# Optimization experiments

Hardware: AMD Instinct MI355X
Metric: run time of the kernel (lower is better)

The kernel has to match this reference:

```python
import jax, jax.numpy as jnp
import numpy as np

N = 20000      # n_nodes
E = 320000     # n_edges (multiple of 4, so _from_coo drops nothing)
D = 512        # embed_dim
H = 8          # num_heads
DK = D // H    # d_k = 64


def setup_inputs() -> dict:
    key = jax.random.key(0)
    ks = jax.random.split(key, 12)
    x = jax.random.normal(ks[0], (N, D), jnp.float32)
    rows = jnp.sort(jax.random.randint(ks[1], (E,), 0, N))
    cols = jax.random.randint(ks[2], (E,), 0, N)
    edge_index = jnp.stack([rows, cols]).astype(jnp.int32)  # [2, E]
    att_bias = jax.random.normal(ks[3], (E, H), jnp.float32)
    s = float(1.0 / np.sqrt(D))  # ~xavier scale
    Wq = jax.random.normal(ks[4], (D, D), jnp.float32) * s
    Wk = jax.random.normal(ks[5], (D, D), jnp.float32) * s
    Wv = jax.random.normal(ks[6], (D, D), jnp.float32) * s
    Wo = jax.random.normal(ks[7], (D, D), jnp.float32) * s
    bq = jnp.zeros((D,), jnp.float32)
    bk = jnp.zeros((D,), jnp.float32)
    bv = jnp.zeros((D,), jnp.float32)
    bo = jnp.zeros((D,), jnp.float32)
    return dict(x=x, edge_index=edge_index, att_bias=att_bias,
                Wq=Wq, bq=bq, Wk=Wk, bk=bk, Wv=Wv, bv=bv, Wo=Wo, bo=bo)


def reference(x, edge_index, att_bias, Wq, bq, Wk, bk, Wv, bv, Wo, bo):
    n = x.shape[0]
    rows, cols = edge_index[0], edge_index[1]
    # per-head projections: [n, H, DK]
    q = (x @ Wq + bq).reshape(n, H, DK)
    k = (x @ Wk + bk).reshape(n, H, DK)
    v = (x @ Wv + bv).reshape(n, H, DK)
    scale = 1.0 / jnp.sqrt(jnp.asarray(DK, x.dtype))
    # masked QK^T on the edge pattern, plus additive bias: [E, H]
    logits = jnp.einsum('ehd,ehd->eh', q[rows] * scale, k[cols]) + att_bias
    # CSR (segment) softmax over each destination row
    row_max = jax.ops.segment_max(logits, rows, num_segments=n)      # [n, H]
    p = jnp.exp(logits - row_max[rows])                              # [E, H]
    denom = jax.ops.segment_sum(p, rows, num_segments=n)            # [n, H]
    att = p / denom[rows]                                            # [E, H]
    # sparse-dense bmm: y[i] = sum_{e: rows[e]=i} att[e] * v[cols[e]]
    y = jax.ops.segment_sum(att[:, :, None] * v[cols], rows, num_segments=n)  # [n, H, DK]
    out = y.reshape(n, H * DK) @ Wo + bo
    return out
```

## Files before the change

### kernel.cpp

```cpp
#include <hip/hip_runtime.h>
#include <hip/hip_bf16.h>

typedef unsigned short ushort_t;
typedef unsigned int uint32;
typedef __attribute__((ext_vector_type(8))) short short8;
typedef __attribute__((ext_vector_type(4))) float floatx4;

#define DEV __device__ __forceinline__

#if defined(__has_builtin)
#if __has_builtin(__builtin_amdgcn_sdot4)
#define HAS_SDOT 1
#endif
#endif
#ifndef HAS_SDOT
#define HAS_SDOT 0
#endif

DEV float b2f(ushort_t u) { return __uint_as_float(((uint32)u) << 16); }
DEV ushort_t f2b(float f) {
  __hip_bfloat16 h = __float2bfloat16(f);
  return __builtin_bit_cast(unsigned short, h);
}
DEV void unpack8(const uint4& u, float* f) {
  f[0] = __uint_as_float(u.x << 16); f[1] = __uint_as_float(u.x & 0xffff0000u);
  f[2] = __uint_as_float(u.y << 16); f[3] = __uint_as_float(u.y & 0xffff0000u);
  f[4] = __uint_as_float(u.z << 16); f[5] = __uint_as_float(u.z & 0xffff0000u);
  f[6] = __uint_as_float(u.w << 16); f[7] = __uint_as_float(u.w & 0xffff0000u);
}
DEV void unpack_i8x8(uint2 u, float* f) {
  f[0] = (float)((int)(u.x << 24) >> 24);
  f[1] = (float)((int)(u.x << 16) >> 24);
  f[2] = (float)((int)(u.x << 8) >> 24);
  f[3] = (float)((int)u.x >> 24);
  f[4] = (float)((int)(u.y << 24) >> 24);
  f[5] = (float)((int)(u.y << 16) >> 24);
  f[6] = (float)((int)(u.y << 8) >> 24);
  f[7] = (float)((int)u.y >> 24);
}

#define GLOAD_LDS(gp, lp) \
  __builtin_amdgcn_global_load_lds((const __attribute__((address_space(1))) uint32*)(gp), \
                                   (__attribute__((address_space(3))) uint32*)(lp), 16, 0, 0)

#define KVROW 1088

DEV int xcd_swz(int wg, int nwg) {
  int q = nwg >> 3, r = nwg & 7;
  int xcd = wg & 7, idx = wg >> 3;
  return (xcd < r ? xcd * (q + 1) : r * (q + 1) + (xcd - r) * q) + idx;
}

__global__ __launch_bounds__(256) void k_detect(const ushort_t* __restrict__ x,
                                                int* __restrict__ flag) {
  __shared__ int red[256];
  int tid = threadIdx.x;
  int wild = 0;
  for (int i = tid; i < 4096; i += 256) {
    uint32 e = (x[i] >> 7) & 0xFFu;
    if (e < 100u || e > 140u) wild++;
  }
  red[tid] = wild;
  __syncthreads();
  for (int s = 128; s > 0; s >>= 1) {
    if (tid < s) red[tid] += red[tid + s];
    __syncthreads();
  }
  if (tid == 0) flag[0] = (red[0] > 400) ? 1 : 0;
}

__global__ __launch_bounds__(256) void k_transpose(
    const void* __restrict__ Wq, const void* __restrict__ Wk,
    const void* __restrict__ Wv, const void* __restrict__ Wo,
    ushort_t* __restrict__ WT4, const int* __restrict__ flagp) {
  __shared__ ushort_t t[32][33];
  int isf32 = *flagp;
  int z = blockIdx.z;
  const void* src = (z == 0) ? Wq : (z == 1) ? Wk : (z == 2) ? Wv : Wo;
  ushort_t* dst = WT4 + (size_t)z * 512 * 512;
  int bx = blockIdx.x, by = blockIdx.y;
  int tx = threadIdx.x, ty = threadIdx.y;
#pragma unroll
  for (int i = 0; i < 4; i++) {
    size_t idx = (size_t)(by * 32 + ty + 8 * i) * 512 + bx * 32 + tx;
    ushort_t v = isf32 ? f2b(((const float*)src)[idx]) : ((const ushort_t*)src)[idx];
    t[ty + 8 * i][tx] = v;
  }
  __syncthreads();
#pragma unroll
  for (int i = 0; i < 4; i++)
    dst[(size_t)(bx * 32 + ty + 8 * i) * 512 + by * 32 + tx] = t[tx][ty + 8 * i];
}

__global__ __launch_bounds__(256) void k_biases(
    const void* __restrict__ bq, const void* __restrict__ bk,
    const void* __restrict__ bv, const void* __restrict__ bo,
    float* __restrict__ biasf, const int* __restrict__ flagp) {
  int i = blockIdx.x * 256 + threadIdx.x;
  if (i >= 2048) return;
  int z = i >> 9, j = i & 511;
  const void* b = (z == 0) ? bq : (z == 1) ? bk : (z == 2) ? bv : bo;
  biasf[i] = (*flagp) ? ((const float*)b)[j] : b2f(((const ushort_t*)b)[j]);
}

__global__ __launch_bounds__(256) void k_convx(
    const void* __restrict__ x, ushort_t* __restrict__ xb, int n8,
    const int* __restrict__ flagp) {
  int i = blockIdx.x * 256 + threadIdx.x;
  if (i >= n8) return;
  if (*flagp) {
    const float* xf = (const float*)x + (size_t)i * 8;
    float4 f0 = ((const float4*)xf)[0];
    float4 f1 = ((const float4*)xf)[1];
    uint4 o;
    o.x = (uint32)f2b(f0.x) | ((uint32)f2b(f0.y) << 16);
    o.y = (uint32)f2b(f0.z) | ((uint32)f2b(f0.w) << 16);
    o.z = (uint32)f2b(f1.x) | ((uint32)f2b(f1.y) << 16);
    o.w = (uint32)f2b(f1.z) | ((uint32)f2b(f1.w) << 16);
    ((uint4*)xb)[i] = o;
  } else {
    ((uint4*)xb)[i] = ((const uint4*)x)[i];
  }
}

__global__ __launch_bounds__(256) void k_convab(
    const void* __restrict__ ab, float* __restrict__ ABc, int n4,
    const int* __restrict__ flagp) {
  if (*flagp) return;
  int i = blockIdx.x * 256 + threadIdx.x;
  if (i >= n4) return;
  uint2 u = ((const uint2*)ab)[i];
  float4 o;
  o.x = __uint_as_float(u.x << 16);
  o.y = __uint_as_float(u.x & 0xffff0000u);
  o.z = __uint_as_float(u.y << 16);
  o.w = __uint_as_float(u.y & 0xffff0000u);
  ((float4*)ABc)[i] = o;
}

__global__ void k_build_rp(const int* __restrict__ rows, int E, int N, int* __restrict__ rp) {
  int i = blockIdx.x * blockDim.x + threadIdx.x;
  if (i > N) return;
  int lo = 0, hi = E;
  while (lo < hi) {
    int mid = (lo + hi) >> 1;
    if (rows[mid] < i) lo = mid + 1; else hi = mid;
  }
  rp[i] = lo;
}

DEV void gemm_body(const ushort_t* __restrict__ A, const ushort_t* __restrict__ BT,
                   const float* __restrict__ bias, void* C,
                   int M, int ldc, float scale, int row0, int by, int mode) {
  __shared__ ushort_t As[2][128 * 32];
  __shared__ ushort_t Bs[2][128 * 32];
  int tid = threadIdx.x;
  int w = tid >> 6, lane = tid & 63;
  int sr = lane >> 2;
  int skz = (((lane & 3) ^ ((lane >> 3) & 3)) * 8);

  floatx4 acc[4][4];
#pragma unroll
  for (int i = 0; i < 4; i++)
#pragma unroll
    for (int j = 0; j < 4; j++)
#pragma unroll
      for (int r = 0; r < 4; r++) acc[i][j][r] = 0.f;

  int lm = lane & 15, quad = lane >> 4;
  int wr = w >> 1, wc = w & 1;
  const int nG = by * 128 + w * 32;

  int rA0 = row0 + w * 32 + sr; if (rA0 >= M) rA0 = M - 1;
  int rA1 = rA0 + 16;          if (rA1 >= M) rA1 = M - 1;
  const ushort_t* gA0 = A + (size_t)rA0 * 512 + skz;
  const ushort_t* gA1 = A + (size_t)rA1 * 512 + skz;
  const ushort_t* gB0 = BT + (size_t)(nG + sr) * 512 + skz;
  const ushort_t* gB1 = BT + (size_t)(nG + 16 + sr) * 512 + skz;

  auto stage = [&](int buf, int k0) {
    GLOAD_LDS(gA0 + k0, &As[buf][(w * 32 + 0) * 32]);
    GLOAD_LDS(gA1 + k0, &As[buf][(w * 32 + 16) * 32]);
    GLOAD_LDS(gB0 + k0, &Bs[buf][(w * 32 + 0) * 32]);
    GLOAD_LDS(gB1 + k0, &Bs[buf][(w * 32 + 16) * 32]);
  };

  int rchunk = (quad ^ ((lm >> 1) & 3)) * 8;

  auto compute = [&](int cur) {
    const ushort_t* pa = &As[cur][(wr * 64 + lm) * 32] + rchunk;
    const ushort_t* pb = &Bs[cur][(wc * 64 + lm) * 32] + rchunk;
    short8 af[4], bfr[4];
#pragma unroll
    for (int t4 = 0; t4 < 4; t4++) {
      af[t4]  = *(const short8*)(pa + t4 * 16 * 32);
      bfr[t4] = *(const short8*)(pb + t4 * 16 * 32);
    }
#pragma unroll
    for (int mt = 0; mt < 4; mt++)
#pragma unroll
      for (int nt = 0; nt < 4; nt++)
        acc[mt][nt] = __builtin_amdgcn_mfma_f32_16x16x32_bf16(af[mt], bfr[nt], acc[mt][nt], 0, 0, 0);
  };

  stage(0, 0);
  for (int ks = 0; ks < 15; ++ks) {
    int cur = ks & 1;
    stage(cur ^ 1, (ks + 1) * 32);
    asm volatile("s_waitcnt vmcnt(4)" ::: "memory");
    __builtin_amdgcn_s_barrier();
    compute(cur);
    asm volatile("s_waitcnt lgkmcnt(0)" ::: "memory");
    __builtin_amdgcn_s_barrier();
  }
  asm volatile("s_waitcnt vmcnt(0)" ::: "memory");
  __builtin_amdgcn_s_barrier();
  compute(1);

  int colB = by * 128 + wc * 64 + lm;
  float bv4[4];
#pragma unroll
  for (int nt = 0; nt < 4; nt++) bv4[nt] = bias[colB + nt * 16];

  if (mode <= 1) {
#pragma unroll
    for (int mt = 0; mt < 4; mt++) {
      int rg0 = row0 + wr * 64 + mt * 16 + quad * 4;
#pragma unroll
      for (int nt = 0; nt < 4; nt++) {
#pragma unroll
        for (int r = 0; r < 4; r++) {
          int rg = rg0 + r;
          if (rg < M) {
            float val = (acc[mt][nt][r] + bv4[nt]) * scale;
            size_t off = (size_t)rg * ldc + colB + nt * 16;
            if (mode == 1) ((float*)C)[off] = val;
            else           ((ushort_t*)C)[off] = f2b(val);
          }
        }
      }
    }
  } else {
    int vslot = (mode == 4);
    int colbase = by * 128 + wc * 64;
    int head = colbase >> 6;
#pragma unroll
    for (int mt = 0; mt < 4; mt++) {
#pragma unroll
      for (int r = 0; r < 4; r++) {
        int rg = row0 + wr * 64 + mt * 16 + quad * 4 + r;
        float v0 = acc[mt][0][r] + bv4[0];
        float v1 = acc[mt][1][r] + bv4[1];
        float v2 = acc[mt][2][r] + bv4[2];
        float v3 = acc[mt][3][r] + bv4[3];
        float am = fmaxf(fmaxf(fabsf(v0), fabsf(v1)), fmaxf(fabsf(v2), fabsf(v3)));
        am = fmaxf(am, __shfl_xor(am, 1));
        am = fmaxf(am, __shfl_xor(am, 2));
        am = fmaxf(am, __shfl_xor(am, 4));
        am = fmaxf(am, __shfl_xor(am, 8));
        am = fmaxf(am, 1e-20f);
        float inv8 = 127.0f / am;
        float sc8 = am * (1.0f / 127.0f);
        if (rg < M) {
          unsigned char* Crow = (unsigned char*)C + (size_t)rg * KVROW;
          unsigned char* bp = Crow + 2 * colbase + 16 * (lm >> 3) + 8 * vslot + (lm & 7);
          bp[ 0] = (unsigned char)(signed char)(int)rintf(v0 * inv8);
          bp[32] = (unsigned char)(signed char)(int)rintf(v1 * inv8);
          bp[64] = (unsigned char)(signed char)(int)rintf(v2 * inv8);
          bp[96] = (unsigned char)(signed char)(int)rintf(v3 * inv8);
          if (lm == 0)
            *(float*)(Crow + 1024 + head * 8 + vslot * 4) = sc8;
        }
      }
    }
  }
}

__global__ __launch_bounds__(256) void k_gemm_qkv(
    const ushort_t* __restrict__ xb, const ushort_t* __restrict__ WT4,
    const float* __restrict__ biasf, ushort_t* Qp, unsigned char* KV8, int M) {
  int swz = xcd_swz(blockIdx.x, gridDim.x);
  int row = swz / 12;
  int sub = swz - row * 12;
  int by = sub & 3, z = sub >> 2;
  const ushort_t* BT = WT4 + (size_t)z * 512 * 512;
  const float* bias = biasf + (size_t)z * 512;
  if (z == 0)
    gemm_body(xb, BT, bias, Qp, M, 512, 0.125f, row * 128, by, 0);
  else
    gemm_body(xb, BT, bias, KV8, M, 0, 1.0f, row * 128, by, z == 1 ? 3 : 4);
}

__global__ __launch_bounds__(256) void k_gemm_out(
    const ushort_t* __restrict__ y, const ushort_t* __restrict__ WT4,
    const float* __restrict__ biasf, void* out, int M,
    const int* __restrict__ flagp) {
  int swz = xcd_swz(blockIdx.x, gridDim.x);
  int row = swz >> 2, by = swz & 3;
  gemm_body(y, WT4 + (size_t)3 * 512 * 512, biasf + 3 * 512, out, M, 512, 1.0f,
            row * 128, by, *flagp);
}

__global__ __launch_bounds__(256) void k_edge(
    ushort_t* Qy, const unsigned char* __restrict__ KV8,
    const void* __restrict__ ab, const float* __restrict__ ABc,
    const int* __restrict__ cols, const int* __restrict__ rp, int Nn,
    const int* __restrict__ flagp) {
  int node = blockIdx.x * 4 + (threadIdx.x >> 6);
  if (node >= Nn) return;
  int lane = threadIdx.x & 63;
  int h8 = lane >> 3;
  const float* abf32 = (*flagp) ? (const float*)ab : ABc;

  uint4 qu = ((const uint4*)(Qy + (size_t)node * 512))[lane];
  float qf[8];
  unpack8(qu, qf);

#if HAS_SDOT
  float qa = 0.f;
#pragma unroll
  for (int j = 0; j < 8; j++) qa = fmaxf(qa, fabsf(qf[j]));
  qa = fmaxf(qa, __shfl_xor(qa, 1));
  qa = fmaxf(qa, __shfl_xor(qa, 2));
  qa = fmaxf(qa, __shfl_xor(qa, 4));
  qa = fmaxf(qa, 1e-20f);
  float qs = qa * (1.0f / 127.0f);
  float qinv = 127.0f / qa;
  int qp0 = 0, qp1 = 0;
#pragma unroll
  for (int j = 0; j < 4; j++) qp0 |= (((int)rintf(qf[j] * qinv)) & 0xFF) << (8 * j);
#pragma unroll
  for (int j = 4; j < 8; j++) qp1 |= (((int)rintf(qf[j] * qinv)) & 0xFF) << (8 * (j - 4));
#endif

  int e0 = rp[node], e1 = rp[node + 1];
  int cnt = e1 - e0;

  float s0 = 0.f, s1 = 0.f;
  float acc0[8], acc1[8];
#pragma unroll
  for (int j = 0; j < 8; j++) { acc0[j] = 0.f; acc1[j] = 0.f; }

  uint4 kvb[4];
  float2 scb[4];
  float abv[4];

  for (int base = 0; base < cnt; base += 64) {
    int rem = cnt - base; if (rem > 64) rem = 64;
    int li = (lane < rem) ? lane : (rem - 1);
    int myc = cols[e0 + base + li];
    const float* abp = abf32 + (size_t)(e0 + base) * 8 + h8;

    auto pref = [&](int t, int slot) {
      int valid = t < rem;
      int c = __builtin_amdgcn_readlane(myc, valid ? t : 0);
      const unsigned char* kvrow = KV8 + (size_t)c * KVROW;
      kvb[slot] = *(const uint4*)(kvrow + lane * 16);
      scb[slot] = *(const float2*)(kvrow + 1024 + h8 * 8);
      float a = abp[(valid ? t : 0) * 8];
      abv[slot] = valid ? a : -1e30f;
    };
    auto consume = [&](int slot, float* acc, float& s) {
#if HAS_SDOT
      int di = __builtin_amdgcn_sdot4(qp0, (int)kvb[slot].x, 0, false);
      di = __builtin_amdgcn_sdot4(qp1, (int)kvb[slot].y, di, false);
      di += __shfl_xor(di, 1);
      di += __shfl_xor(di, 2);
      di += __shfl_xor(di, 4);
      float logit = fminf(fmaf((float)di * qs, scb[slot].x, abv[slot]), 80.f);
#else
      float kf[8];
      uint2 ku; ku.x = kvb[slot].x; ku.y = kvb[slot].y;
      unpack_i8x8(ku, kf);
      float d = 0.f;
#pragma unroll
      for (int j = 0; j < 8; j++) d = fmaf(qf[j], kf[j], d);
      d += __shfl_xor(d, 1);
      d += __shfl_xor(d, 2);
      d += __shfl_xor(d, 4);
      float logit = fminf(fmaf(d, scb[slot].x, abv[slot]), 80.f);
#endif
      float pw = __expf(logit);
      s += pw;
      float pwv = pw * scb[slot].y;
      float vf[8];
      uint2 vu; vu.x = kvb[slot].z; vu.y = kvb[slot].w;
      unpack_i8x8(vu, vf);
#pragma unroll
      for (int j = 0; j < 8; j++) acc[j] = fmaf(pwv, vf[j], acc[j]);
    };

    pref(0, 0); pref(1, 1); pref(2, 2); pref(3, 3);
    int iters = (rem + 3) >> 2;
    for (int it = 0; it < iters; ++it) {
      int nt = it * 4 + 4;
      consume(0, acc0, s0); pref(nt + 0, 0);
      consume(1, acc1, s1); pref(nt + 1, 1);
      consume(2, acc0, s0); pref(nt + 2, 2);
      consume(3, acc1, s1); pref(nt + 3, 3);
    }
  }

  float s = s0 + s1;
  float inv = (cnt > 0 && s > 0.f) ? 1.f / s : 0.f;
  ushort_t hb[8];
#pragma unroll
  for (int j = 0; j < 8; j++) hb[j] = f2b((acc0[j] + acc1[j]) * inv);
  uint4 uh;
  uh.x = (uint32)hb[0] | ((uint32)hb[1] << 16);
  uh.y = (uint32)hb[2] | ((uint32)hb[3] << 16);
  uh.z = (uint32)hb[4] | ((uint32)hb[5] << 16);
  uh.w = (uint32)hb[6] | ((uint32)hb[7] << 16);
  ((uint4*)(Qy + (size_t)node * 512))[lane] = uh;
}

extern "C" void kernel_launch(void* const* d_in, const int* in_sizes, int n_in,
                              void* d_out, int out_size, void* d_ws, size_t ws_size,
                              hipStream_t stream) {
  const void* x  = d_in[0];
  const int* ei  = (const int*)d_in[1];
  const void* ab = d_in[2];
  const void* Wq = d_in[3];
  const void* bq = d_in[4];
  const void* Wk = d_in[5];
  const void* bk = d_in[6];
  const void* Wv = d_in[7];
  const void* bv = d_in[8];
  const void* Wo = d_in[9];
  const void* bo = d_in[10];

  const int D = 512;
  int M = in_sizes[0] / D;
  int E = in_sizes[1] / 2;
  const int* rows = ei;
  const int* cols = ei + E;

  char* p = (char*)d_ws;
  size_t off = 0;
  auto carve = [&](size_t bytes) -> void* {
    off = (off + 255) & ~(size_t)255;
    void* r = p + off;
    off += bytes;
    return r;
  };
  int* flag          = (int*)carve(4);
  ushort_t* WT4      = (ushort_t*)carve((size_t)4 * 512 * 512 * 2);
  float* biasf       = (float*)carve((size_t)4 * 512 * 4);
  ushort_t* xb       = (ushort_t*)carve((size_t)M * 512 * 2);
  ushort_t* Qp       = (ushort_t*)carve((size_t)M * 512 * 2);
  unsigned char* KV8 = (unsigned char*)carve((size_t)M * KVROW);
  int* rp            = (int*)carve((size_t)(M + 1) * 4);
  (void)ws_size;
  float* ABc = (float*)xb;

  k_detect<<<1, 256, 0, stream>>>((const ushort_t*)x, flag);
  k_transpose<<<dim3(16, 16, 4), dim3(32, 8), 0, stream>>>(Wq, Wk, Wv, Wo, WT4, flag);
  k_biases<<<8, 256, 0, stream>>>(bq, bk, bv, bo, biasf, flag);
  int n8 = M * 512 / 8;
  k_convx<<<(n8 + 255) / 256, 256, 0, stream>>>(x, xb, n8, flag);
  k_build_rp<<<(M + 1 + 255) / 256, 256, 0, stream>>>(rows, E, M, rp);

  int rb = (M + 127) / 128;
  k_gemm_qkv<<<rb * 12, 256, 0, stream>>>(xb, WT4, biasf, Qp, KV8, M);
  int n4 = E * 8 / 4;
  k_convab<<<(n4 + 255) / 256, 256, 0, stream>>>(ab, ABc, n4, flag);
  k_edge<<<(M + 3) / 4, 256, 0, stream>>>(Qp, KV8, ab, ABc, cols, rp, M, flag);
  k_gemm_out<<<rb * 4, 256, 0, stream>>>(Qp, WT4, biasf, d_out, M, flag);
}
```

Baseline: 268.7 us.

## Enlarge GEMM tiles to 256x256 with 512-thread blocks and 64-wide K steps

Replaces the 128x128x32 GEMM body with a 256x256x64 tile computed by 8 waves, each owning a 128x64 sub-tile. LDS layout gets a new XOR swizzle, and the MFMA loops are wrapped in s_setprio. The aim is more reuse per staged byte and fewer barriers per K. In exchange, LDS rises to 128KB per block, register pressure grows, and the grids shrink (about 474 QKV blocks and 158 out-GEMM blocks), which may leave CUs underfilled.

After: 268.5 us. About the same (-0.1%).

```diff
diff --git a/kernel.cpp b/kernel.cpp
--- a/kernel.cpp
+++ b/kernel.cpp
@@ -149,83 +149,96 @@
   rp[i] = lo;
 }
 
-DEV void gemm_body(const ushort_t* __restrict__ A, const ushort_t* __restrict__ BT,
-                   const float* __restrict__ bias, void* C,
-                   int M, int ldc, float scale, int row0, int by, int mode) {
-  __shared__ ushort_t As[2][128 * 32];
-  __shared__ ushort_t Bs[2][128 * 32];
+DEV void gemm_body256(const ushort_t* __restrict__ A, const ushort_t* __restrict__ BT,
+                      const float* __restrict__ bias, void* C,
+                      int M, int ldc, float scale, int row0, int by, int mode) {
+  __shared__ ushort_t Ab[2][256 * 64];
+  __shared__ ushort_t Bb[2][256 * 64];
   int tid = threadIdx.x;
   int w = tid >> 6, lane = tid & 63;
-  int sr = lane >> 2;
-  int skz = (((lane & 3) ^ ((lane >> 3) & 3)) * 8);
-
-  floatx4 acc[4][4];
-#pragma unroll
-  for (int i = 0; i < 4; i++)
+  int lm = lane & 15, quad = lane >> 4;
+  int wr = w >> 2, wc = w & 3;
+
+  asm volatile("s_waitcnt vmcnt(0)" ::: "memory");
+
+  int clog8 = ((lane & 7) ^ (lane >> 3)) * 8;
+  int arow[4], brow[4];
+#pragma unroll
+  for (int i = 0; i < 4; i++) {
+    int r = row0 + i * 64 + w * 8 + (lane >> 3);
+    arow[i] = (r < M) ? r : (M - 1);
+    brow[i] = by * 256 + i * 64 + w * 8 + (lane >> 3);
+  }
+
+  floatx4 acc[8][4];
+#pragma unroll
+  for (int i = 0; i < 8; i++)
 #pragma unroll
     for (int j = 0; j < 4; j++)
 #pragma unroll
       for (int r = 0; r < 4; r++) acc[i][j][r] = 0.f;
 
-  int lm = lane & 15, quad = lane >> 4;
-  int wr = w >> 1, wc = w & 1;
-  const int nG = by * 128 + w * 32;
-
-  int rA0 = row0 + w * 32 + sr; if (rA0 >= M) rA0 = M - 1;
-  int rA1 = rA0 + 16;          if (rA1 >= M) rA1 = M - 1;
-  const ushort_t* gA0 = A + (size_t)rA0 * 512 + skz;
-  const ushort_t* gA1 = A + (size_t)rA1 * 512 + skz;
-  const ushort_t* gB0 = BT + (size_t)(nG + sr) * 512 + skz;
-  const ushort_t* gB1 = BT + (size_t)(nG + 16 + sr) * 512 + skz;
-
-  auto stage = [&](int buf, int k0) {
-    GLOAD_LDS(gA0 + k0, &As[buf][(w * 32 + 0) * 32]);
-    GLOAD_LDS(gA1 + k0, &As[buf][(w * 32 + 16) * 32]);
-    GLOAD_LDS(gB0 + k0, &Bs[buf][(w * 32 + 0) * 32]);
-    GLOAD_LDS(gB1 + k0, &Bs[buf][(w * 32 + 16) * 32]);
+  auto stage = [&](int buf, int kt) {
+    int k0 = kt * 64 + clog8;
+#pragma unroll
+    for (int i = 0; i < 4; i++)
+      GLOAD_LDS(A + (size_t)arow[i] * 512 + k0, &Ab[buf][(i * 64 + w * 8) * 64]);
+#pragma unroll
+    for (int i = 0; i < 4; i++)
+      GLOAD_LDS(BT + (size_t)brow[i] * 512 + k0, &Bb[buf][(i * 64 + w * 8) * 64]);
   };
 
-  int rchunk = (quad ^ ((lm >> 1) & 3)) * 8;
+  int ph0 = ((0 + quad) ^ (lm & 7)) * 8;
+  int ph1 = ((4 + quad) ^ (lm & 7)) * 8;
 
   auto compute = [&](int cur) {
-    const ushort_t* pa = &As[cur][(wr * 64 + lm) * 32] + rchunk;
-    const ushort_t* pb = &Bs[cur][(wc * 64 + lm) * 32] + rchunk;
-    short8 af[4], bfr[4];
-#pragma unroll
-    for (int t4 = 0; t4 < 4; t4++) {
-      af[t4]  = *(const short8*)(pa + t4 * 16 * 32);
-      bfr[t4] = *(const short8*)(pb + t4 * 16 * 32);
-    }
-#pragma unroll
-    for (int mt = 0; mt < 4; mt++)
-#pragma unroll
-      for (int nt = 0; nt < 4; nt++)
-        acc[mt][nt] = __builtin_amdgcn_mfma_f32_16x16x32_bf16(af[mt], bfr[nt], acc[mt][nt], 0, 0, 0);
+#pragma unroll
+    for (int kk = 0; kk < 2; kk++) {
+      int ph = kk ? ph1 : ph0;
+      const ushort_t* pa = &Ab[cur][(wr * 128 + lm) * 64] + ph;
+      const ushort_t* pb = &Bb[cur][(wc * 64 + lm) * 64] + ph;
+      short8 af[8], bf[4];
+#pragma unroll
+      for (int nt = 0; nt < 4; nt++) bf[nt] = *(const short8*)(pb + nt * 16 * 64);
+#pragma unroll
+      for (int mt = 0; mt < 8; mt++) af[mt] = *(const short8*)(pa + mt * 16 * 64);
+      __builtin_amdgcn_s_setprio(1);
+#pragma unroll
+      for (int mt = 0; mt < 8; mt++)
+#pragma unroll
+        for (int nt = 0; nt < 4; nt++)
+          acc[mt][nt] = __builtin_amdgcn_mfma_f32_16x16x32_bf16(af[mt], bf[nt], acc[mt][nt], 0, 0, 0);
+      __builtin_amdgcn_s_setprio(0);
+    }
   };
 
   stage(0, 0);
-  for (int ks = 0; ks < 15; ++ks) {
-    int cur = ks & 1;
-    stage(cur ^ 1, (ks + 1) * 32);
-    asm volatile("s_waitcnt vmcnt(4)" ::: "memory");
+#pragma unroll 1
+  for (int kt = 0; kt < 8; ++kt) {
+    int cur = kt & 1;
+    if (kt < 7) {
+      stage(cur ^ 1, kt + 1);
+      asm volatile("s_waitcnt vmcnt(8)" ::: "memory");
+    } else {
+      asm volatile("s_waitcnt vmcnt(0)" ::: "memory");
+    }
     __builtin_amdgcn_s_barrier();
     compute(cur);
-    asm volatile("s_waitcnt lgkmcnt(0)" ::: "memory");
-    __builtin_amdgcn_s_barrier();
-  }
-  asm volatile("s_waitcnt vmcnt(0)" ::: "memory");
-  __builtin_amdgcn_s_barrier();
-  compute(1);
-
-  int colB = by * 128 + wc * 64 + lm;
+    if (kt < 7) {
+      asm volatile("s_waitcnt lgkmcnt(0)" ::: "memory");
+      __builtin_amdgcn_s_barrier();
+    }
+  }
+
+  int colB = by * 256 + wc * 64 + lm;
   float bv4[4];
 #pragma unroll
   for (int nt = 0; nt < 4; nt++) bv4[nt] = bias[colB + nt * 16];
 
   if (mode <= 1) {
 #pragma unroll
-    for (int mt = 0; mt < 4; mt++) {
-      int rg0 = row0 + wr * 64 + mt * 16 + quad * 4;
+    for (int mt = 0; mt < 8; mt++) {
+      int rg0 = row0 + wr * 128 + mt * 16 + quad * 4;
 #pragma unroll
       for (int nt = 0; nt < 4; nt++) {
 #pragma unroll
@@ -242,13 +255,12 @@
     }
   } else {
     int vslot = (mode == 4);
-    int colbase = by * 128 + wc * 64;
-    int head = colbase >> 6;
-#pragma unroll
-    for (int mt = 0; mt < 4; mt++) {
+    int head = (by * 256 + wc * 64) >> 6;
+#pragma unroll
+    for (int mt = 0; mt < 8; mt++) {
 #pragma unroll
       for (int r = 0; r < 4; r++) {
-        int rg = row0 + wr * 64 + mt * 16 + quad * 4 + r;
+        int rg = row0 + wr * 128 + mt * 16 + quad * 4 + r;
         float v0 = acc[mt][0][r] + bv4[0];
         float v1 = acc[mt][1][r] + bv4[1];
         float v2 = acc[mt][2][r] + bv4[2];
@@ -263,7 +275,7 @@
         float sc8 = am * (1.0f / 127.0f);
         if (rg < M) {
           unsigned char* Crow = (unsigned char*)C + (size_t)rg * KVROW;
-          unsigned char* bp = Crow + 2 * colbase + 16 * (lm >> 3) + 8 * vslot + (lm & 7);
+          unsigned char* bp = Crow + head * 128 + (lm >> 3) * 16 + 8 * vslot + (lm & 7);
           bp[ 0] = (unsigned char)(signed char)(int)rintf(v0 * inv8);
           bp[32] = (unsigned char)(signed char)(int)rintf(v1 * inv8);
           bp[64] = (unsigned char)(signed char)(int)rintf(v2 * inv8);
@@ -276,29 +288,30 @@
   }
 }
 
-__global__ __launch_bounds__(256) void k_gemm_qkv(
+__global__ __launch_bounds__(512, 2) void k_gemm_qkv(
     const ushort_t* __restrict__ xb, const ushort_t* __restrict__ WT4,
     const float* __restrict__ biasf, ushort_t* Qp, unsigned char* KV8, int M) {
   int swz = xcd_swz(blockIdx.x, gridDim.x);
-  int row = swz / 12;
-  int sub = swz - row * 12;
-  int by = sub & 3, z = sub >> 2;
+  int row = swz / 6;
+  int sub = swz - row * 6;
+  int by = sub & 1, z = sub >> 1;
   const ushort_t* BT = WT4 + (size_t)z * 512 * 512;
   const float* bias = biasf + (size_t)z * 512;
   if (z == 0)
-    gemm_body(xb, BT, bias, Qp, M, 512, 0.125f, row * 128, by, 0);
+    gemm_body256(xb, BT, bias, Qp, M, 512, 0.125f, row * 256, by, 0);
   else
-    gemm_body(xb, BT, bias, KV8, M, 0, 1.0f, row * 128, by, z == 1 ? 3 : 4);
-}
-
-__global__ __launch_bounds__(256) void k_gemm_out(
+    gemm_body256(xb, BT, bias, KV8, M, 0, 1.0f, row * 256, by, z == 1 ? 3 : 4);
+}
+
+__global__ __launch_bounds__(512, 2) void k_gemm_out(
     const ushort_t* __restrict__ y, const ushort_t* __restrict__ WT4,
     const float* __restrict__ biasf, void* out, int M,
     const int* __restrict__ flagp) {
+  int mode = *flagp;
   int swz = xcd_swz(blockIdx.x, gridDim.x);
-  int row = swz >> 2, by = swz & 3;
-  gemm_body(y, WT4 + (size_t)3 * 512 * 512, biasf + 3 * 512, out, M, 512, 1.0f,
-            row * 128, by, *flagp);
+  int row = swz >> 1, by = swz & 1;
+  gemm_body256(y, WT4 + (size_t)3 * 512 * 512, biasf + 3 * 512, out, M, 512, 1.0f,
+               row * 256, by, mode);
 }
 
 __global__ __launch_bounds__(256) void k_edge(
@@ -460,10 +473,10 @@
   k_convx<<<(n8 + 255) / 256, 256, 0, stream>>>(x, xb, n8, flag);
   k_build_rp<<<(M + 1 + 255) / 256, 256, 0, stream>>>(rows, E, M, rp);
 
-  int rb = (M + 127) / 128;
-  k_gemm_qkv<<<rb * 12, 256, 0, stream>>>(xb, WT4, biasf, Qp, KV8, M);
+  int rt = (M + 255) / 256;
+  k_gemm_qkv<<<rt * 6, 512, 0, stream>>>(xb, WT4, biasf, Qp, KV8, M);
   int n4 = E * 8 / 4;
   k_convab<<<(n4 + 255) / 256, 256, 0, stream>>>(ab, ABc, n4, flag);
   k_edge<<<(M + 3) / 4, 256, 0, stream>>>(Qp, KV8, ab, ABc, cols, rp, M, flag);
-  k_gemm_out<<<rb * 4, 256, 0, stream>>>(Qp, WT4, biasf, d_out, M, flag);
-}
+  k_gemm_out<<<rt * 2, 512, 0, stream>>>(Qp, WT4, biasf, d_out, M, flag);
+}
```
